# Optimization experiments

Hardware: AMD Instinct MI355X
Metric: run time of the kernel (lower is better)

## Reference

```python
import jax, jax.numpy as jnp
import numpy as np

N, E, IN, HID, OUT, HEADS = 50000, 800000, 256, 256, 128, 4
HC = HID // HEADS  # 64
EPS = 1e-5


def layer_norm(x, g, b):
    mu = x.mean(-1, keepdims=True)
    var = ((x - mu) ** 2).mean(-1, keepdims=True)
    return (x - mu) * jax.lax.rsqrt(var + EPS) * g + b


def gat_conv(x, W, a_s, a_d, bias, src, dst, heads, C, concat):
    # PyG GATConv (eval mode): linear -> per-edge LeakyReLU attention ->
    # segment softmax over destination -> scatter-sum aggregation -> bias
    n = x.shape[0]
    xw = (x @ W).reshape(n, heads, C)                     # [N,H,C]
    al_s = jnp.einsum('nhc,hc->nh', xw, a_s)              # [N,H]
    al_d = jnp.einsum('nhc,hc->nh', xw, a_d)
    e = jax.nn.leaky_relu(al_s[src] + al_d[dst], 0.2)     # [Etot,H]
    m = jax.ops.segment_max(e, dst, num_segments=n)
    ex = jnp.exp(e - m[dst])
    denom = jax.ops.segment_sum(ex, dst, num_segments=n)
    alpha = ex / denom[dst]                               # [Etot,H]
    out = jax.ops.segment_sum(xw[src] * alpha[:, :, None], dst, num_segments=n)
    out = out.reshape(n, heads * C) if concat else out.mean(axis=1)
    return out + bias


def setup_inputs() -> dict:
    key = jax.random.key(0)
    ks = jax.random.split(key, 20)
    s = 0.05
    return {
        'x': jax.random.normal(ks[0], (N, IN), jnp.float32),
        'edge_index': jax.random.randint(ks[1], (2, E), 0, N, jnp.int64),
        'Wp': jax.random.normal(ks[2], (IN, HID), jnp.float32) * s,
        'bp': jnp.zeros((HID,), jnp.float32),
        'W0': jax.random.normal(ks[3], (HID, HEADS * HC), jnp.float32) * s,
        'as0': jax.random.normal(ks[4], (HEADS, HC), jnp.float32) * s,
        'ad0': jax.random.normal(ks[5], (HEADS, HC), jnp.float32) * s,
        'b0': jnp.zeros((HID,), jnp.float32),
        'W1': jax.random.normal(ks[6], (HID, OUT), jnp.float32) * s,
        'as1': jax.random.normal(ks[7], (1, OUT), jnp.float32) * s,
        'ad1': jax.random.normal(ks[8], (1, OUT), jnp.float32) * s,
        'b1': jnp.zeros((OUT,), jnp.float32),
        'g0': jnp.ones((HID,), jnp.float32),
        'be0': jnp.zeros((HID,), jnp.float32),
        'g1': jnp.ones((OUT,), jnp.float32),
        'be1': jnp.zeros((OUT,), jnp.float32),
        'Wo': jax.random.normal(ks[9], (OUT, OUT), jnp.float32) * s,
        'bo': jnp.zeros((OUT,), jnp.float32),
    }


def reference(x, edge_index, Wp, bp, W0, as0, ad0, b0, W1, as1, ad1, b1,
              g0, be0, g1, be1, Wo, bo):
    n = x.shape[0]
    # add self loops (PyG GATConv default)
    ar = jnp.arange(n, dtype=edge_index.dtype)
    src = jnp.concatenate([edge_index[0], ar])
    dst = jnp.concatenate([edge_index[1], ar])

    h = jax.nn.relu(x @ Wp + bp)
    # layer 0: multi-head, concat, LN + residual + relu
    h1 = gat_conv(h, W0, as0, ad0, b0, src, dst, HEADS, HC, True)
    h1 = layer_norm(h1, g0, be0)
    h1 = jax.nn.relu(h1 + h)
    # layer 1: single head, no concat, LN (no residual: shape check still passes
    # only when identity is not None; here identity is None for last layer)
    h2 = gat_conv(h1, W1, as1, ad1, b1, src, dst, 1, OUT, False)
    h2 = layer_norm(h2, g1, be1)
    out = h2 @ Wo + bo
    out = out / jnp.maximum(jnp.linalg.norm(out, axis=-1, keepdims=True), 1e-12)
    return out
```

## Files before the change

### kernel.cpp

```cpp
#include <hip/hip_runtime.h>
#include <hip/hip_bf16.h>

typedef __bf16 bf16x8 __attribute__((ext_vector_type(8)));
typedef __bf16 bf16x4 __attribute__((ext_vector_type(4)));
typedef __bf16 bf16x2 __attribute__((ext_vector_type(2)));
typedef float f32x4 __attribute__((ext_vector_type(4)));

__device__ __forceinline__ float getf(const void* p, size_t i, int isf32){
  return isf32 ? ((const float*)p)[i]
               : __bfloat162float(((const __hip_bfloat16*)p)[i]);
}
__device__ __forceinline__ int getedge(const void* p, long long idx, int is64, int n){
  long long v = is64 ? ((const long long*)p)[idx] : (long long)((const int*)p)[idx];
  v = v < 0 ? 0 : (v >= n ? (long long)(n - 1) : v);
  return (int)v;
}

__device__ __forceinline__ float bfly_sum(float v){
#pragma unroll
  for (int m = 32; m > 0; m >>= 1) v += __shfl_xor(v, m, 64);
  return v;
}

__device__ __forceinline__ float bf_lo(unsigned u){ return __uint_as_float(u << 16); }
__device__ __forceinline__ float bf_hi(unsigned u){ return __uint_as_float(u & 0xffff0000u); }

__global__ __launch_bounds__(256) void detect_kernel(const void* x, const void* ei,
                                                     int* flags){
  __shared__ int cnt_sane, cnt_odd;
  int t = threadIdx.x;
  if (t == 0){ cnt_sane = 0; cnt_odd = 0; }
  __syncthreads();
  int sane = 0;
  for (int i = t; i < 4096; i += 256){
    float v = __bfloat162float(((const __hip_bfloat16*)x)[i]);
    if (fabsf(v) < 16.f) sane++;
  }
  atomicAdd(&cnt_sane, sane);
  int odd = 0;
  for (int i = t; i < 512; i += 256){
    if (((const int*)ei)[2 * i + 1] != 0) odd++;
  }
  atomicAdd(&cnt_odd, odd);
  __syncthreads();
  if (t == 0){
    flags[0] = (cnt_sane < 3900) ? 1 : 0;
    flags[1] = (cnt_odd == 0) ? 1 : 0;
  }
}

__global__ __launch_bounds__(256) void count_kernel(const void* __restrict__ ei, long long E,
                                                    int n, const int* __restrict__ flags,
                                                    int* __restrict__ cnt){
  int i = blockIdx.x * blockDim.x + threadIdx.x;
  if (i < E){
    int d = getedge(ei, E + i, flags[1], n);
    atomicAdd(&cnt[d], 1);
  }
}

__global__ __launch_bounds__(1024) void scan_kernel(const int* __restrict__ cnt, int* __restrict__ off,
                                                    int* __restrict__ pos, int n){
  __shared__ int wsum[16];
  __shared__ int carry_s;
  int tid = threadIdx.x, lane = tid & 63, wv = tid >> 6;
  if (tid == 0) carry_s = 0;
  __syncthreads();
  for (int base = 0; base < n; base += 4096){
    int i0 = base + tid * 4;
    int v0 = 0, v1 = 0, v2 = 0, v3 = 0;
    if (i0 + 3 < n){
      int4 q = *(const int4*)(cnt + i0);
      v0 = q.x; v1 = q.y; v2 = q.z; v3 = q.w;
    } else {
      if (i0 < n)     v0 = cnt[i0];
      if (i0 + 1 < n) v1 = cnt[i0 + 1];
      if (i0 + 2 < n) v2 = cnt[i0 + 2];
      if (i0 + 3 < n) v3 = cnt[i0 + 3];
    }
    int s4 = v0 + v1 + v2 + v3;
    int s = s4;
#pragma unroll
    for (int o = 1; o < 64; o <<= 1){ int t = __shfl_up(s, o, 64); if (lane >= o) s += t; }
    if (lane == 63) wsum[wv] = s;
    __syncthreads();
    int wo = 0;
    for (int w = 0; w < wv; w++) wo += wsum[w];
    int carry = carry_s;
    int e0 = carry + wo + s - s4;
    if (i0 + 3 < n){
      int4 o4; o4.x = e0; o4.y = e0 + v0; o4.z = e0 + v0 + v1; o4.w = e0 + v0 + v1 + v2;
      *(int4*)(off + i0) = o4;
      *(int4*)(pos + i0) = o4;
    } else {
      if (i0 < n)     { off[i0] = e0;               pos[i0] = e0; }
      if (i0 + 1 < n) { off[i0+1] = e0+v0;          pos[i0+1] = e0+v0; }
      if (i0 + 2 < n) { off[i0+2] = e0+v0+v1;       pos[i0+2] = e0+v0+v1; }
      if (i0 + 3 < n) { off[i0+3] = e0+v0+v1+v2;    pos[i0+3] = e0+v0+v1+v2; }
    }
    __syncthreads();
    if (tid == 0){
      int tot = 0;
      for (int w = 0; w < 16; w++) tot += wsum[w];
      carry_s = carry + tot;
    }
    __syncthreads();
  }
  if (tid == 0) off[n] = carry_s;
}

__global__ __launch_bounds__(256) void fill_kernel(const void* __restrict__ ei, long long E,
                                                   int n, const int* __restrict__ flags,
                                                   int* __restrict__ pos, int* __restrict__ bsrc){
  int i = blockIdx.x * blockDim.x + threadIdx.x;
  if (i < E){
    int d = getedge(ei, E + i, flags[1], n);
    int s = getedge(ei, i, flags[1], n);
    int p = atomicAdd(&pos[d], 1);
    bsrc[p] = s;
  }
}

__global__ __launch_bounds__(256) void transpose_all_kernel(
    const void* __restrict__ Wp, const void* __restrict__ W0,
    const void* __restrict__ W1, const void* __restrict__ Wo,
    const int* __restrict__ flags,
    __hip_bfloat16* __restrict__ btp, __hip_bfloat16* __restrict__ bt0,
    __hip_bfloat16* __restrict__ bt1, __hip_bfloat16* __restrict__ bto)
{
  int f0 = flags[0];
  int o = blockIdx.x * 256 + threadIdx.x;
  const void* W; __hip_bfloat16* B; int K, N, loc;
  if (o < 65536)       { W = Wp; B = btp; K = 256; N = 256; loc = o; }
  else if (o < 131072) { W = W0; B = bt0; K = 256; N = 256; loc = o - 65536; }
  else if (o < 163840) { W = W1; B = bt1; K = 256; N = 128; loc = o - 131072; }
  else if (o < 180224) { W = Wo; B = bto; K = 128; N = 128; loc = o - 163840; }
  else return;
  int nn = loc / K, kk = loc - nn * K;
  B[loc] = __float2bfloat16(getf(W, (size_t)kk * N + nn, f0));
}

__device__ __forceinline__ bf16x8 pk8(f32x4 u, f32x4 w){
  bf16x8 r;
  r[0] = (__bf16)u.x; r[1] = (__bf16)u.y; r[2] = (__bf16)u.z; r[3] = (__bf16)u.w;
  r[4] = (__bf16)w.x; r[5] = (__bf16)w.y; r[6] = (__bf16)w.z; r[7] = (__bf16)w.w;
  return r;
}

template<int AMODE, bool OUTF, bool OUTB, bool RELU, bool BIAS, bool NORM, int ALMODE>
__global__ __launch_bounds__(256) void gemm_direct_kernel(
    const void* __restrict__ A, const __hip_bfloat16* __restrict__ Bt,
    const void* __restrict__ bias, const void* __restrict__ a_s, const void* __restrict__ a_d,
    const int* __restrict__ flags,
    float* __restrict__ Cf, __hip_bfloat16* __restrict__ Cb,
    float* __restrict__ als, float* __restrict__ ald,
    int M, int N, int K)
{
  const int f0 = flags[0];
  const bool af32 = (AMODE == 1) && (f0 != 0);
  int t = threadIdx.x;
  int wave = t >> 6, lane = t & 63;
  int q = lane >> 4, mi = lane & 15;
  int bm = blockIdx.x * 128 + wave * 32;
  int bn = blockIdx.y * 128;

  int r0 = min(bm + mi, M - 1);
  int r1 = min(bm + 16 + mi, M - 1);

  f32x4 acc[2][8] = {};

  if (af32){
    const float* Af = (const float*)A;
    const float* p0 = Af + (size_t)r0 * K + q * 8;
    const float* p1 = Af + (size_t)r1 * K + q * 8;
#pragma unroll 2
    for (int k0 = 0; k0 < K; k0 += 32){
      f32x4 u0 = *(const f32x4*)(p0 + k0);
      f32x4 w0 = *(const f32x4*)(p0 + k0 + 4);
      f32x4 u1 = *(const f32x4*)(p1 + k0);
      f32x4 w1 = *(const f32x4*)(p1 + k0 + 4);
      bf16x8 a0 = pk8(u0, w0);
      bf16x8 a1 = pk8(u1, w1);
#pragma unroll
      for (int nt = 0; nt < 8; nt++){
        bf16x8 b = *(const bf16x8*)(Bt + (size_t)(bn + nt * 16 + mi) * K + k0 + q * 8);
        acc[0][nt] = __builtin_amdgcn_mfma_f32_16x16x32_bf16(a0, b, acc[0][nt], 0, 0, 0);
        acc[1][nt] = __builtin_amdgcn_mfma_f32_16x16x32_bf16(a1, b, acc[1][nt], 0, 0, 0);
      }
    }
  } else {
    const __hip_bfloat16* Ab = (const __hip_bfloat16*)A;
    const __hip_bfloat16* p0 = Ab + (size_t)r0 * K + q * 8;
    const __hip_bfloat16* p1 = Ab + (size_t)r1 * K + q * 8;
#pragma unroll 2
    for (int k0 = 0; k0 < K; k0 += 32){
      bf16x8 a0 = *(const bf16x8*)(p0 + k0);
      bf16x8 a1 = *(const bf16x8*)(p1 + k0);
#pragma unroll
      for (int nt = 0; nt < 8; nt++){
        bf16x8 b = *(const bf16x8*)(Bt + (size_t)(bn + nt * 16 + mi) * K + k0 + q * 8);
        acc[0][nt] = __builtin_amdgcn_mfma_f32_16x16x32_bf16(a0, b, acc[0][nt], 0, 0, 0);
        acc[1][nt] = __builtin_amdgcn_mfma_f32_16x16x32_bf16(a1, b, acc[1][nt], 0, 0, 0);
      }
    }
  }

  float bv[8], asv[8], adv[8];
  if (BIAS){
#pragma unroll
    for (int nt = 0; nt < 8; nt++) bv[nt] = getf(bias, bn + nt * 16 + mi, f0);
  }
  if (ALMODE != 0){
#pragma unroll
    for (int nt = 0; nt < 8; nt++){
      asv[nt] = getf(a_s, bn + nt * 16 + mi, f0);
      adv[nt] = getf(a_d, bn + nt * 16 + mi, f0);
    }
  }
#pragma unroll
  for (int mt = 0; mt < 2; mt++){
#pragma unroll
    for (int r = 0; r < 4; r++){
      int row = bm + mt * 16 + q * 4 + r;
      float vv[8];
#pragma unroll
      for (int nt = 0; nt < 8; nt++){
        float v = acc[mt][nt][r];
        if (BIAS) v += bv[nt];
        if (RELU) v = fmaxf(v, 0.f);
        vv[nt] = v;
      }
      if (NORM){
        float ss = 0.f;
#pragma unroll
        for (int nt = 0; nt < 8; nt++) ss += vv[nt] * vv[nt];
        ss += __shfl_xor(ss, 1, 64);
        ss += __shfl_xor(ss, 2, 64);
        ss += __shfl_xor(ss, 4, 64);
        ss += __shfl_xor(ss, 8, 64);
        float inv = 1.f / fmaxf(sqrtf(ss), 1e-12f);
#pragma unroll
        for (int nt = 0; nt < 8; nt++) vv[nt] *= inv;
      }
      if (ALMODE == 1){
        float ps0 = 0.f, pd0 = 0.f, ps1 = 0.f, pd1 = 0.f;
#pragma unroll
        for (int nt = 0; nt < 4; nt++){ ps0 += vv[nt] * asv[nt]; pd0 += vv[nt] * adv[nt]; }
#pragma unroll
        for (int nt = 4; nt < 8; nt++){ ps1 += vv[nt] * asv[nt]; pd1 += vv[nt] * adv[nt]; }
#pragma unroll
        for (int m = 1; m < 16; m <<= 1){
          ps0 += __shfl_xor(ps0, m, 64); pd0 += __shfl_xor(pd0, m, 64);
          ps1 += __shfl_xor(ps1, m, 64); pd1 += __shfl_xor(pd1, m, 64);
        }
        if ((lane & 15) == 0 && row < M){
          int h0 = blockIdx.y * 2;
          als[(size_t)row * 4 + h0]     = ps0; ald[(size_t)row * 4 + h0]     = pd0;
          als[(size_t)row * 4 + h0 + 1] = ps1; ald[(size_t)row * 4 + h0 + 1] = pd1;
        }
      } else if (ALMODE == 2){
        float ps = 0.f, pd = 0.f;
#pragma unroll
        for (int nt = 0; nt < 8; nt++){ ps += vv[nt] * asv[nt]; pd += vv[nt] * adv[nt]; }
#pragma unroll
        for (int m = 1; m < 16; m <<= 1){
          ps += __shfl_xor(ps, m, 64); pd += __shfl_xor(pd, m, 64);
        }
        if ((lane & 15) == 0 && row < M){ als[row] = ps; ald[row] = pd; }
      }
      if (row < M){
#pragma unroll
        for (int nt = 0; nt < 8; nt++){
          int col = bn + nt * 16 + mi;
          size_t idx = (size_t)row * N + col;
          if (OUTF) Cf[idx] = vv[nt];
          if (OUTB) Cb[idx] = __float2bfloat16(vv[nt]);
        }
      }
    }
  }
}

#define FMA4(U, W) do { \
  m0 += (W) * bf_lo((U).x); m1 += (W) * bf_hi((U).x); \
  m2 += (W) * bf_lo((U).y); m3 += (W) * bf_hi((U).y); \
} while (0)

#define FMA2(U, W) do { \
  m0 += (W) * bf_lo(U); m1 += (W) * bf_hi(U); \
} while (0)

__global__ __launch_bounds__(256) void gather0_kernel(
    const __hip_bfloat16* __restrict__ xw, const float* __restrict__ als, const float* __restrict__ ald,
    const int* __restrict__ bsrc, const int* __restrict__ off,
    const void* __restrict__ bias, const void* __restrict__ gamma,
    const void* __restrict__ beta, const int* __restrict__ flags,
    __hip_bfloat16* __restrict__ hbuf, int n)
{
  int f0 = flags[0];
  int t = threadIdx.x, wv = t >> 6, lane = t & 63;
  int i = blockIdx.x * 4 + wv;
  if (i >= n) return;
  int head = lane >> 4;
  int ch = lane * 4;
  int e0 = off[i], jend = off[i + 1];

  float m0 = 0.f, m1 = 0.f, m2 = 0.f, m3 = 0.f;
  float aldi = ald[(size_t)i * 4 + head];

  float se = als[(size_t)i * 4 + head] + aldi;
  se = (se > 0.f) ? se : 0.2f * se;
  float eself = __expf(se);
  {
    uint2 u = *(const uint2*)(xw + (size_t)i * 256 + ch);
    FMA4(u, eself);
  }
  float wacc = eself;

  int j = e0;
  for (; j + 7 < jend; j += 8){
    int s0 = bsrc[j],     s1 = bsrc[j + 1], s2 = bsrc[j + 2], s3 = bsrc[j + 3];
    int s4 = bsrc[j + 4], s5 = bsrc[j + 5], s6 = bsrc[j + 6], s7 = bsrc[j + 7];
    float l0 = als[(size_t)s0 * 4 + head] + aldi;
    float l1 = als[(size_t)s1 * 4 + head] + aldi;
    float l2 = als[(size_t)s2 * 4 + head] + aldi;
    float l3 = als[(size_t)s3 * 4 + head] + aldi;
    float l4 = als[(size_t)s4 * 4 + head] + aldi;
    float l5 = als[(size_t)s5 * 4 + head] + aldi;
    float l6 = als[(size_t)s6 * 4 + head] + aldi;
    float l7 = als[(size_t)s7 * 4 + head] + aldi;
    l0 = (l0 > 0.f) ? l0 : 0.2f * l0;  l1 = (l1 > 0.f) ? l1 : 0.2f * l1;
    l2 = (l2 > 0.f) ? l2 : 0.2f * l2;  l3 = (l3 > 0.f) ? l3 : 0.2f * l3;
    l4 = (l4 > 0.f) ? l4 : 0.2f * l4;  l5 = (l5 > 0.f) ? l5 : 0.2f * l5;
    l6 = (l6 > 0.f) ? l6 : 0.2f * l6;  l7 = (l7 > 0.f) ? l7 : 0.2f * l7;
    float w0 = __expf(l0), w1 = __expf(l1), w2 = __expf(l2), w3 = __expf(l3);
    float w4 = __expf(l4), w5 = __expf(l5), w6 = __expf(l6), w7 = __expf(l7);
    uint2 U0 = *(const uint2*)(xw + (size_t)s0 * 256 + ch);
    uint2 U1 = *(const uint2*)(xw + (size_t)s1 * 256 + ch);
    uint2 U2 = *(const uint2*)(xw + (size_t)s2 * 256 + ch);
    uint2 U3 = *(const uint2*)(xw + (size_t)s3 * 256 + ch);
    uint2 U4 = *(const uint2*)(xw + (size_t)s4 * 256 + ch);
    uint2 U5 = *(const uint2*)(xw + (size_t)s5 * 256 + ch);
    uint2 U6 = *(const uint2*)(xw + (size_t)s6 * 256 + ch);
    uint2 U7 = *(const uint2*)(xw + (size_t)s7 * 256 + ch);
    wacc += w0 + w1 + w2 + w3 + w4 + w5 + w6 + w7;
    FMA4(U0, w0); FMA4(U1, w1); FMA4(U2, w2); FMA4(U3, w3);
    FMA4(U4, w4); FMA4(U5, w5); FMA4(U6, w6); FMA4(U7, w7);
  }
  for (; j + 3 < jend; j += 4){
    int s0 = bsrc[j], s1 = bsrc[j + 1], s2 = bsrc[j + 2], s3 = bsrc[j + 3];
    float l0 = als[(size_t)s0 * 4 + head] + aldi;
    float l1 = als[(size_t)s1 * 4 + head] + aldi;
    float l2 = als[(size_t)s2 * 4 + head] + aldi;
    float l3 = als[(size_t)s3 * 4 + head] + aldi;
    l0 = (l0 > 0.f) ? l0 : 0.2f * l0;  l1 = (l1 > 0.f) ? l1 : 0.2f * l1;
    l2 = (l2 > 0.f) ? l2 : 0.2f * l2;  l3 = (l3 > 0.f) ? l3 : 0.2f * l3;
    float w0 = __expf(l0), w1 = __expf(l1), w2 = __expf(l2), w3 = __expf(l3);
    uint2 U0 = *(const uint2*)(xw + (size_t)s0 * 256 + ch);
    uint2 U1 = *(const uint2*)(xw + (size_t)s1 * 256 + ch);
    uint2 U2 = *(const uint2*)(xw + (size_t)s2 * 256 + ch);
    uint2 U3 = *(const uint2*)(xw + (size_t)s3 * 256 + ch);
    wacc += w0 + w1 + w2 + w3;
    FMA4(U0, w0); FMA4(U1, w1); FMA4(U2, w2); FMA4(U3, w3);
  }
  for (; j < jend; j++){
    int s0 = bsrc[j];
    float l0 = als[(size_t)s0 * 4 + head] + aldi;
    l0 = (l0 > 0.f) ? l0 : 0.2f * l0;
    float w0 = __expf(l0);
    uint2 U0 = *(const uint2*)(xw + (size_t)s0 * 256 + ch);
    wacc += w0;
    FMA4(U0, w0);
  }

  float rl = 1.f / wacc;
  float v0 = m0 * rl + getf(bias, ch + 0, f0);
  float v1 = m1 * rl + getf(bias, ch + 1, f0);
  float v2 = m2 * rl + getf(bias, ch + 2, f0);
  float v3 = m3 * rl + getf(bias, ch + 3, f0);

  float mu = bfly_sum(v0 + v1 + v2 + v3) * (1.f / 256.f);
  float d0 = v0 - mu, d1 = v1 - mu, d2 = v2 - mu, d3 = v3 - mu;
  float var = bfly_sum(d0 * d0 + d1 * d1 + d2 * d2 + d3 * d3) * (1.f / 256.f);
  float rs = rsqrtf(var + 1e-5f);

  bf16x4 rb = *(const bf16x4*)(hbuf + (size_t)i * 256 + ch);
  float y0 = fmaxf(d0 * rs * getf(gamma, ch + 0, f0) + getf(beta, ch + 0, f0) + (float)rb[0], 0.f);
  float y1 = fmaxf(d1 * rs * getf(gamma, ch + 1, f0) + getf(beta, ch + 1, f0) + (float)rb[1], 0.f);
  float y2 = fmaxf(d2 * rs * getf(gamma, ch + 2, f0) + getf(beta, ch + 2, f0) + (float)rb[2], 0.f);
  float y3 = fmaxf(d3 * rs * getf(gamma, ch + 3, f0) + getf(beta, ch + 3, f0) + (float)rb[3], 0.f);

  bf16x4 o;
  o[0] = (__bf16)y0; o[1] = (__bf16)y1; o[2] = (__bf16)y2; o[3] = (__bf16)y3;
  *(bf16x4*)(hbuf + (size_t)i * 256 + ch) = o;
}

__global__ __launch_bounds__(256) void gather1_kernel(
    const __hip_bfloat16* __restrict__ xw, const float* __restrict__ als, const float* __restrict__ ald,
    const int* __restrict__ bsrc, const int* __restrict__ off,
    const void* __restrict__ bias, const void* __restrict__ gamma,
    const void* __restrict__ beta, const int* __restrict__ flags,
    __hip_bfloat16* __restrict__ outb, int n)
{
  int f0 = flags[0];
  int t = threadIdx.x, wv = t >> 6, lane = t & 63;
  int i = blockIdx.x * 4 + wv;
  if (i >= n) return;
  int ch = lane * 2;
  int e0 = off[i], jend = off[i + 1];

  float m0 = 0.f, m1 = 0.f;

  float aldi = ald[i];
  float se = als[i] + aldi;
  se = (se > 0.f) ? se : 0.2f * se;
  float eself = __expf(se);
  {
    unsigned u = *(const unsigned*)(xw + (size_t)i * 128 + ch);
    FMA2(u, eself);
  }
  float wacc = eself;

  int j = e0;
  for (; j + 7 < jend; j += 8){
    int s0 = bsrc[j],     s1 = bsrc[j + 1], s2 = bsrc[j + 2], s3 = bsrc[j + 3];
    int s4 = bsrc[j + 4], s5 = bsrc[j + 5], s6 = bsrc[j + 6], s7 = bsrc[j + 7];
    float l0 = als[s0] + aldi, l1 = als[s1] + aldi, l2 = als[s2] + aldi, l3 = als[s3] + aldi;
    float l4 = als[s4] + aldi, l5 = als[s5] + aldi, l6 = als[s6] + aldi, l7 = als[s7] + aldi;
    l0 = (l0 > 0.f) ? l0 : 0.2f * l0;  l1 = (l1 > 0.f) ? l1 : 0.2f * l1;
    l2 = (l2 > 0.f) ? l2 : 0.2f * l2;  l3 = (l3 > 0.f) ? l3 : 0.2f * l3;
    l4 = (l4 > 0.f) ? l4 : 0.2f * l4;  l5 = (l5 > 0.f) ? l5 : 0.2f * l5;
    l6 = (l6 > 0.f) ? l6 : 0.2f * l6;  l7 = (l7 > 0.f) ? l7 : 0.2f * l7;
    float w0 = __expf(l0), w1 = __expf(l1), w2 = __expf(l2), w3 = __expf(l3);
    float w4 = __expf(l4), w5 = __expf(l5), w6 = __expf(l6), w7 = __expf(l7);
    unsigned U0 = *(const unsigned*)(xw + (size_t)s0 * 128 + ch);
    unsigned U1 = *(const unsigned*)(xw + (size_t)s1 * 128 + ch);
    unsigned U2 = *(const unsigned*)(xw + (size_t)s2 * 128 + ch);
    unsigned U3 = *(const unsigned*)(xw + (size_t)s3 * 128 + ch);
    unsigned U4 = *(const unsigned*)(xw + (size_t)s4 * 128 + ch);
    unsigned U5 = *(const unsigned*)(xw + (size_t)s5 * 128 + ch);
    unsigned U6 = *(const unsigned*)(xw + (size_t)s6 * 128 + ch);
    unsigned U7 = *(const unsigned*)(xw + (size_t)s7 * 128 + ch);
    wacc += w0 + w1 + w2 + w3 + w4 + w5 + w6 + w7;
    FMA2(U0, w0); FMA2(U1, w1); FMA2(U2, w2); FMA2(U3, w3);
    FMA2(U4, w4); FMA2(U5, w5); FMA2(U6, w6); FMA2(U7, w7);
  }
  for (; j + 3 < jend; j += 4){
    int s0 = bsrc[j], s1 = bsrc[j + 1], s2 = bsrc[j + 2], s3 = bsrc[j + 3];
    float l0 = als[s0] + aldi, l1 = als[s1] + aldi, l2 = als[s2] + aldi, l3 = als[s3] + aldi;
    l0 = (l0 > 0.f) ? l0 : 0.2f * l0;  l1 = (l1 > 0.f) ? l1 : 0.2f * l1;
    l2 = (l2 > 0.f) ? l2 : 0.2f * l2;  l3 = (l3 > 0.f) ? l3 : 0.2f * l3;
    float w0 = __expf(l0), w1 = __expf(l1), w2 = __expf(l2), w3 = __expf(l3);
    unsigned U0 = *(const unsigned*)(xw + (size_t)s0 * 128 + ch);
    unsigned U1 = *(const unsigned*)(xw + (size_t)s1 * 128 + ch);
    unsigned U2 = *(const unsigned*)(xw + (size_t)s2 * 128 + ch);
    unsigned U3 = *(const unsigned*)(xw + (size_t)s3 * 128 + ch);
    wacc += w0 + w1 + w2 + w3;
    FMA2(U0, w0); FMA2(U1, w1); FMA2(U2, w2); FMA2(U3, w3);
  }
  for (; j < jend; j++){
    int s0 = bsrc[j];
    float l0 = als[s0] + aldi;
    l0 = (l0 > 0.f) ? l0 : 0.2f * l0;
    float w0 = __expf(l0);
    unsigned U0 = *(const unsigned*)(xw + (size_t)s0 * 128 + ch);
    wacc += w0;
    FMA2(U0, w0);
  }

  float rl = 1.f / wacc;
  float v0 = m0 * rl + getf(bias, ch + 0, f0);
  float v1 = m1 * rl + getf(bias, ch + 1, f0);

  float mu = bfly_sum(v0 + v1) * (1.f / 128.f);
  float d0 = v0 - mu, d1 = v1 - mu;
  float var = bfly_sum(d0 * d0 + d1 * d1) * (1.f / 128.f);
  float rs = rsqrtf(var + 1e-5f);

  float y0 = d0 * rs * getf(gamma, ch + 0, f0) + getf(beta, ch + 0, f0);
  float y1 = d1 * rs * getf(gamma, ch + 1, f0) + getf(beta, ch + 1, f0);

  bf16x2 o;
  o[0] = (__bf16)y0; o[1] = (__bf16)y1;
  *(bf16x2*)(outb + (size_t)i * 128 + ch) = o;
}

extern "C" void kernel_launch(void* const* d_in, const int* in_sizes, int n_in,
                              void* d_out, int out_size, void* d_ws, size_t ws_size,
                              hipStream_t stream)
{
  const void* x   = d_in[0];
  const void* ei  = d_in[1];
  const void* Wp  = d_in[2];
  const void* bp  = d_in[3];
  const void* W0  = d_in[4];
  const void* as0 = d_in[5];
  const void* ad0 = d_in[6];
  const void* b0  = d_in[7];
  const void* W1  = d_in[8];
  const void* as1 = d_in[9];
  const void* ad1 = d_in[10];
  const void* b1  = d_in[11];
  const void* g0  = d_in[12];
  const void* be0 = d_in[13];
  const void* g1  = d_in[14];
  const void* be1 = d_in[15];
  const void* Wo  = d_in[16];
  const void* bo  = d_in[17];
  float* outp = (float*)d_out;

  const int n = in_sizes[0] / 256;
  const int E = in_sizes[1] / 2;

  char* w = (char*)d_ws;
  size_t SZ = (size_t)n * 256 * sizeof(float);
  __hip_bfloat16* h_bf  = (__hip_bfloat16*)w;
  __hip_bfloat16* xw_bf = (__hip_bfloat16*)(w + SZ / 2);
  char* p = w + SZ;
  int* flags = (int*)p; p += 64;
  float* als0 = (float*)p; p += (size_t)n * 4 * sizeof(float);
  float* ald0 = (float*)p; p += (size_t)n * 4 * sizeof(float);
  float* als1 = (float*)p; p += (size_t)n * sizeof(float);
  float* ald1 = (float*)p; p += (size_t)n * sizeof(float);
  int* cnt    = (int*)p; p += (size_t)n * sizeof(int);
  int* offb   = (int*)p; p += (size_t)(n + 4) * sizeof(int);
  int* pos    = (int*)p; p += (size_t)n * sizeof(int);
  int* bsrc   = (int*)p; p += (size_t)E * sizeof(int);
  p = (char*)(((uintptr_t)p + 15) & ~(uintptr_t)15);
  __hip_bfloat16* bt_p = (__hip_bfloat16*)p; p += (size_t)256 * 256 * 2;
  __hip_bfloat16* bt_0 = (__hip_bfloat16*)p; p += (size_t)256 * 256 * 2;
  __hip_bfloat16* bt_1 = (__hip_bfloat16*)p; p += (size_t)128 * 256 * 2;
  __hip_bfloat16* bt_o = (__hip_bfloat16*)p; p += (size_t)128 * 128 * 2;

  detect_kernel<<<1, 256, 0, stream>>>(x, ei, flags);

  transpose_all_kernel<<<704, 256, 0, stream>>>(Wp, W0, W1, Wo, flags, bt_p, bt_0, bt_1, bt_o);

  (void)hipMemsetAsync(cnt, 0, (size_t)n * sizeof(int), stream);
  count_kernel<<<(E + 255) / 256, 256, 0, stream>>>(ei, E, n, flags, cnt);
  scan_kernel<<<1, 1024, 0, stream>>>(cnt, offb, pos, n);
  fill_kernel<<<(E + 255) / 256, 256, 0, stream>>>(ei, E, n, flags, pos, bsrc);

  int gm = (n + 127) / 128;
  int gn4 = (n + 3) / 4;

  gemm_direct_kernel<1, false, true, true, true, false, 0><<<dim3(gm, 2), 256, 0, stream>>>(
      x, bt_p, bp, nullptr, nullptr, flags, nullptr, h_bf, nullptr, nullptr, n, 256, 256);
  gemm_direct_kernel<0, false, true, false, false, false, 1><<<dim3(gm, 2), 256, 0, stream>>>(
      h_bf, bt_0, nullptr, as0, ad0, flags, nullptr, xw_bf, als0, ald0, n, 256, 256);
  gather0_kernel<<<gn4, 256, 0, stream>>>(xw_bf, als0, ald0, bsrc, offb, b0, g0, be0,
                                          flags, h_bf, n);
  gemm_direct_kernel<0, false, true, false, false, false, 2><<<dim3(gm, 1), 256, 0, stream>>>(
      h_bf, bt_1, nullptr, as1, ad1, flags, nullptr, xw_bf, als1, ald1, n, 128, 256);
  gather1_kernel<<<gn4, 256, 0, stream>>>(xw_bf, als1, ald1, bsrc, offb, b1, g1, be1,
                                          flags, h_bf, n);
  gemm_direct_kernel<0, true, false, false, true, true, 0><<<dim3(gm, 1), 256, 0, stream>>>(
      h_bf, bt_o, bo, nullptr, nullptr, flags, outp, nullptr, nullptr, nullptr, n, 128, 128);
}
```

Before: 485.1 us.

## Parallelize CSR offset scan across blocks and widen GEMM N-tile to full width

```diff
diff --git a/kernel.cpp b/kernel.cpp
--- a/kernel.cpp
+++ b/kernel.cpp
@@ -59,54 +59,79 @@
   }
 }
 
-__global__ __launch_bounds__(1024) void scan_kernel(const int* __restrict__ cnt, int* __restrict__ off,
-                                                    int* __restrict__ pos, int n){
+__global__ __launch_bounds__(1024) void scan_part_kernel(const int* __restrict__ cnt, int n,
+                                                         int* __restrict__ bsum){
   __shared__ int wsum[16];
-  __shared__ int carry_s;
   int tid = threadIdx.x, lane = tid & 63, wv = tid >> 6;
-  if (tid == 0) carry_s = 0;
+  int i0 = blockIdx.x * 4096 + tid * 4;
+  int s4 = 0;
+  if (i0 + 3 < n){
+    int4 q = *(const int4*)(cnt + i0);
+    s4 = q.x + q.y + q.z + q.w;
+  } else {
+    if (i0 < n)     s4 += cnt[i0];
+    if (i0 + 1 < n) s4 += cnt[i0 + 1];
+    if (i0 + 2 < n) s4 += cnt[i0 + 2];
+    if (i0 + 3 < n) s4 += cnt[i0 + 3];
+  }
+  int s = s4;
+#pragma unroll
+  for (int o = 1; o < 64; o <<= 1) s += __shfl_xor(s, o, 64);
+  if (lane == 0) wsum[wv] = s;
   __syncthreads();
-  for (int base = 0; base < n; base += 4096){
-    int i0 = base + tid * 4;
-    int v0 = 0, v1 = 0, v2 = 0, v3 = 0;
-    if (i0 + 3 < n){
-      int4 q = *(const int4*)(cnt + i0);
-      v0 = q.x; v1 = q.y; v2 = q.z; v3 = q.w;
-    } else {
-      if (i0 < n)     v0 = cnt[i0];
-      if (i0 + 1 < n) v1 = cnt[i0 + 1];
-      if (i0 + 2 < n) v2 = cnt[i0 + 2];
-      if (i0 + 3 < n) v3 = cnt[i0 + 3];
-    }
-    int s4 = v0 + v1 + v2 + v3;
-    int s = s4;
-#pragma unroll
-    for (int o = 1; o < 64; o <<= 1){ int t = __shfl_up(s, o, 64); if (lane >= o) s += t; }
-    if (lane == 63) wsum[wv] = s;
-    __syncthreads();
-    int wo = 0;
-    for (int w = 0; w < wv; w++) wo += wsum[w];
-    int carry = carry_s;
-    int e0 = carry + wo + s - s4;
-    if (i0 + 3 < n){
-      int4 o4; o4.x = e0; o4.y = e0 + v0; o4.z = e0 + v0 + v1; o4.w = e0 + v0 + v1 + v2;
-      *(int4*)(off + i0) = o4;
-      *(int4*)(pos + i0) = o4;
-    } else {
-      if (i0 < n)     { off[i0] = e0;               pos[i0] = e0; }
-      if (i0 + 1 < n) { off[i0+1] = e0+v0;          pos[i0+1] = e0+v0; }
-      if (i0 + 2 < n) { off[i0+2] = e0+v0+v1;       pos[i0+2] = e0+v0+v1; }
-      if (i0 + 3 < n) { off[i0+3] = e0+v0+v1+v2;    pos[i0+3] = e0+v0+v1+v2; }
-    }
-    __syncthreads();
-    if (tid == 0){
-      int tot = 0;
-      for (int w = 0; w < 16; w++) tot += wsum[w];
-      carry_s = carry + tot;
-    }
-    __syncthreads();
-  }
-  if (tid == 0) off[n] = carry_s;
+  if (tid == 0){
+    int tot = 0;
+    for (int w = 0; w < 16; w++) tot += wsum[w];
+    bsum[blockIdx.x] = tot;
+  }
+}
+
+__global__ __launch_bounds__(64) void scan_top_kernel(int* __restrict__ bsum, int nb,
+                                                      int* __restrict__ off, int n){
+  int lane = threadIdx.x;
+  int v = (lane < nb) ? bsum[lane] : 0;
+  int s = v;
+#pragma unroll
+  for (int o = 1; o < 64; o <<= 1){ int t = __shfl_up(s, o, 64); if (lane >= o) s += t; }
+  if (lane < nb) bsum[lane] = s - v;
+  if (lane == 63) off[n] = s;
+}
+
+__global__ __launch_bounds__(1024) void scan_fin_kernel(const int* __restrict__ cnt, int n,
+                                                        const int* __restrict__ bsum,
+                                                        int* __restrict__ off, int* __restrict__ pos){
+  __shared__ int wsum[16];
+  int tid = threadIdx.x, lane = tid & 63, wv = tid >> 6;
+  int i0 = blockIdx.x * 4096 + tid * 4;
+  int v0 = 0, v1 = 0, v2 = 0, v3 = 0;
+  if (i0 + 3 < n){
+    int4 q = *(const int4*)(cnt + i0);
+    v0 = q.x; v1 = q.y; v2 = q.z; v3 = q.w;
+  } else {
+    if (i0 < n)     v0 = cnt[i0];
+    if (i0 + 1 < n) v1 = cnt[i0 + 1];
+    if (i0 + 2 < n) v2 = cnt[i0 + 2];
+    if (i0 + 3 < n) v3 = cnt[i0 + 3];
+  }
+  int s4 = v0 + v1 + v2 + v3;
+  int s = s4;
+#pragma unroll
+  for (int o = 1; o < 64; o <<= 1){ int t = __shfl_up(s, o, 64); if (lane >= o) s += t; }
+  if (lane == 63) wsum[wv] = s;
+  __syncthreads();
+  int wo = 0;
+  for (int w = 0; w < wv; w++) wo += wsum[w];
+  int e0 = bsum[blockIdx.x] + wo + s - s4;
+  if (i0 + 3 < n){
+    int4 o4; o4.x = e0; o4.y = e0 + v0; o4.z = e0 + v0 + v1; o4.w = e0 + v0 + v1 + v2;
+    *(int4*)(off + i0) = o4;
+    *(int4*)(pos + i0) = o4;
+  } else {
+    if (i0 < n)     { off[i0] = e0;               pos[i0] = e0; }
+    if (i0 + 1 < n) { off[i0+1] = e0+v0;          pos[i0+1] = e0+v0; }
+    if (i0 + 2 < n) { off[i0+2] = e0+v0+v1;       pos[i0+2] = e0+v0+v1; }
+    if (i0 + 3 < n) { off[i0+3] = e0+v0+v1+v2;    pos[i0+3] = e0+v0+v1+v2; }
+  }
 }
 
 __global__ __launch_bounds__(256) void fill_kernel(const void* __restrict__ ei, long long E,
@@ -147,7 +172,7 @@
   return r;
 }
 
-template<int AMODE, bool OUTF, bool OUTB, bool RELU, bool BIAS, bool NORM, int ALMODE>
+template<int AMODE, bool OUTF, bool OUTB, bool RELU, bool BIAS, bool NORM, int ALMODE, int NT>
 __global__ __launch_bounds__(256) void gemm_direct_kernel(
     const void* __restrict__ A, const __hip_bfloat16* __restrict__ Bt,
     const void* __restrict__ bias, const void* __restrict__ a_s, const void* __restrict__ a_d,
@@ -162,57 +187,54 @@
   int wave = t >> 6, lane = t & 63;
   int q = lane >> 4, mi = lane & 15;
   int bm = blockIdx.x * 128 + wave * 32;
-  int bn = blockIdx.y * 128;
+  int bn = blockIdx.y * (NT * 16);
 
   int r0 = min(bm + mi, M - 1);
   int r1 = min(bm + 16 + mi, M - 1);
 
-  f32x4 acc[2][8] = {};
-
-  if (af32){
-    const float* Af = (const float*)A;
-    const float* p0 = Af + (size_t)r0 * K + q * 8;
-    const float* p1 = Af + (size_t)r1 * K + q * 8;
+  f32x4 acc[2][NT] = {};
+
+  const float* pf0 = (const float*)A + (size_t)r0 * K + q * 8;
+  const float* pf1 = (const float*)A + (size_t)r1 * K + q * 8;
+  const __hip_bfloat16* pb0 = (const __hip_bfloat16*)A + (size_t)r0 * K + q * 8;
+  const __hip_bfloat16* pb1 = (const __hip_bfloat16*)A + (size_t)r1 * K + q * 8;
+
+  auto kstep = [&](int k0){
+    bf16x8 a0, a1;
+    if (af32){
+      f32x4 u0 = *(const f32x4*)(pf0 + k0);
+      f32x4 w0 = *(const f32x4*)(pf0 + k0 + 4);
+      f32x4 u1 = *(const f32x4*)(pf1 + k0);
+      f32x4 w1 = *(const f32x4*)(pf1 + k0 + 4);
+      a0 = pk8(u0, w0);
+      a1 = pk8(u1, w1);
+    } else {
+      a0 = *(const bf16x8*)(pb0 + k0);
+      a1 = *(const bf16x8*)(pb1 + k0);
+    }
+#pragma unroll
+    for (int nt = 0; nt < NT; nt++){
+      bf16x8 b = *(const bf16x8*)(Bt + (size_t)(bn + nt * 16 + mi) * K + k0 + q * 8);
+      acc[0][nt] = __builtin_amdgcn_mfma_f32_16x16x32_bf16(a0, b, acc[0][nt], 0, 0, 0);
+      acc[1][nt] = __builtin_amdgcn_mfma_f32_16x16x32_bf16(a1, b, acc[1][nt], 0, 0, 0);
+    }
+  };
+  if constexpr (NT == 8){
 #pragma unroll 2
-    for (int k0 = 0; k0 < K; k0 += 32){
-      f32x4 u0 = *(const f32x4*)(p0 + k0);
-      f32x4 w0 = *(const f32x4*)(p0 + k0 + 4);
-      f32x4 u1 = *(const f32x4*)(p1 + k0);
-      f32x4 w1 = *(const f32x4*)(p1 + k0 + 4);
-      bf16x8 a0 = pk8(u0, w0);
-      bf16x8 a1 = pk8(u1, w1);
-#pragma unroll
-      for (int nt = 0; nt < 8; nt++){
-        bf16x8 b = *(const bf16x8*)(Bt + (size_t)(bn + nt * 16 + mi) * K + k0 + q * 8);
-        acc[0][nt] = __builtin_amdgcn_mfma_f32_16x16x32_bf16(a0, b, acc[0][nt], 0, 0, 0);
-        acc[1][nt] = __builtin_amdgcn_mfma_f32_16x16x32_bf16(a1, b, acc[1][nt], 0, 0, 0);
-      }
-    }
+    for (int k0 = 0; k0 < K; k0 += 32) kstep(k0);
   } else {
-    const __hip_bfloat16* Ab = (const __hip_bfloat16*)A;
-    const __hip_bfloat16* p0 = Ab + (size_t)r0 * K + q * 8;
-    const __hip_bfloat16* p1 = Ab + (size_t)r1 * K + q * 8;
-#pragma unroll 2
-    for (int k0 = 0; k0 < K; k0 += 32){
-      bf16x8 a0 = *(const bf16x8*)(p0 + k0);
-      bf16x8 a1 = *(const bf16x8*)(p1 + k0);
-#pragma unroll
-      for (int nt = 0; nt < 8; nt++){
-        bf16x8 b = *(const bf16x8*)(Bt + (size_t)(bn + nt * 16 + mi) * K + k0 + q * 8);
-        acc[0][nt] = __builtin_amdgcn_mfma_f32_16x16x32_bf16(a0, b, acc[0][nt], 0, 0, 0);
-        acc[1][nt] = __builtin_amdgcn_mfma_f32_16x16x32_bf16(a1, b, acc[1][nt], 0, 0, 0);
-      }
-    }
-  }
-
-  float bv[8], asv[8], adv[8];
+#pragma unroll 1
+    for (int k0 = 0; k0 < K; k0 += 32) kstep(k0);
+  }
+
+  float bv[NT], asv[NT], adv[NT];
   if (BIAS){
 #pragma unroll
-    for (int nt = 0; nt < 8; nt++) bv[nt] = getf(bias, bn + nt * 16 + mi, f0);
+    for (int nt = 0; nt < NT; nt++) bv[nt] = getf(bias, bn + nt * 16 + mi, f0);
   }
   if (ALMODE != 0){
 #pragma unroll
-    for (int nt = 0; nt < 8; nt++){
+    for (int nt = 0; nt < NT; nt++){
       asv[nt] = getf(a_s, bn + nt * 16 + mi, f0);
       adv[nt] = getf(a_d, bn + nt * 16 + mi, f0);
     }
@@ -222,9 +244,9 @@
 #pragma unroll
     for (int r = 0; r < 4; r++){
       int row = bm + mt * 16 + q * 4 + r;
-      float vv[8];
-#pragma unroll
-      for (int nt = 0; nt < 8; nt++){
+      float vv[NT];
+#pragma unroll
+      for (int nt = 0; nt < NT; nt++){
         float v = acc[mt][nt][r];
         if (BIAS) v += bv[nt];
         if (RELU) v = fmaxf(v, 0.f);
@@ -233,35 +255,41 @@
       if (NORM){
         float ss = 0.f;
 #pragma unroll
-        for (int nt = 0; nt < 8; nt++) ss += vv[nt] * vv[nt];
+        for (int nt = 0; nt < NT; nt++) ss += vv[nt] * vv[nt];
         ss += __shfl_xor(ss, 1, 64);
         ss += __shfl_xor(ss, 2, 64);
         ss += __shfl_xor(ss, 4, 64);
         ss += __shfl_xor(ss, 8, 64);
         float inv = 1.f / fmaxf(sqrtf(ss), 1e-12f);
 #pragma unroll
-        for (int nt = 0; nt < 8; nt++) vv[nt] *= inv;
+        for (int nt = 0; nt < NT; nt++) vv[nt] *= inv;
       }
       if (ALMODE == 1){
-        float ps0 = 0.f, pd0 = 0.f, ps1 = 0.f, pd1 = 0.f;
-#pragma unroll
-        for (int nt = 0; nt < 4; nt++){ ps0 += vv[nt] * asv[nt]; pd0 += vv[nt] * adv[nt]; }
-#pragma unroll
-        for (int nt = 4; nt < 8; nt++){ ps1 += vv[nt] * asv[nt]; pd1 += vv[nt] * adv[nt]; }
-#pragma unroll
-        for (int m = 1; m < 16; m <<= 1){
-          ps0 += __shfl_xor(ps0, m, 64); pd0 += __shfl_xor(pd0, m, 64);
-          ps1 += __shfl_xor(ps1, m, 64); pd1 += __shfl_xor(pd1, m, 64);
+        float ps[4] = {0.f, 0.f, 0.f, 0.f}, pd[4] = {0.f, 0.f, 0.f, 0.f};
+#pragma unroll
+        for (int h = 0; h < 4; h++){
+#pragma unroll
+          for (int g = 0; g < 4; g++){
+            ps[h] += vv[h * 4 + g] * asv[h * 4 + g];
+            pd[h] += vv[h * 4 + g] * adv[h * 4 + g];
+          }
+#pragma unroll
+          for (int m = 1; m < 16; m <<= 1){
+            ps[h] += __shfl_xor(ps[h], m, 64);
+            pd[h] += __shfl_xor(pd[h], m, 64);
+          }
         }
         if ((lane & 15) == 0 && row < M){
-          int h0 = blockIdx.y * 2;
-          als[(size_t)row * 4 + h0]     = ps0; ald[(size_t)row * 4 + h0]     = pd0;
-          als[(size_t)row * 4 + h0 + 1] = ps1; ald[(size_t)row * 4 + h0 + 1] = pd1;
+#pragma unroll
+          for (int h = 0; h < 4; h++){
+            als[(size_t)row * 4 + h] = ps[h];
+            ald[(size_t)row * 4 + h] = pd[h];
+          }
         }
       } else if (ALMODE == 2){
         float ps = 0.f, pd = 0.f;
 #pragma unroll
-        for (int nt = 0; nt < 8; nt++){ ps += vv[nt] * asv[nt]; pd += vv[nt] * adv[nt]; }
+        for (int nt = 0; nt < NT; nt++){ ps += vv[nt] * asv[nt]; pd += vv[nt] * adv[nt]; }
 #pragma unroll
         for (int m = 1; m < 16; m <<= 1){
           ps += __shfl_xor(ps, m, 64); pd += __shfl_xor(pd, m, 64);
@@ -270,7 +298,7 @@
       }
       if (row < M){
 #pragma unroll
-        for (int nt = 0; nt < 8; nt++){
+        for (int nt = 0; nt < NT; nt++){
           int col = bn + nt * 16 + mi;
           size_t idx = (size_t)row * N + col;
           if (OUTF) Cf[idx] = vv[nt];
@@ -525,6 +553,7 @@
   int* cnt    = (int*)p; p += (size_t)n * sizeof(int);
   int* offb   = (int*)p; p += (size_t)(n + 4) * sizeof(int);
   int* pos    = (int*)p; p += (size_t)n * sizeof(int);
+  int* bsum   = (int*)p; p += 64 * sizeof(int);
   int* bsrc   = (int*)p; p += (size_t)E * sizeof(int);
   p = (char*)(((uintptr_t)p + 15) & ~(uintptr_t)15);
   __hip_bfloat16* bt_p = (__hip_bfloat16*)p; p += (size_t)256 * 256 * 2;
@@ -538,22 +567,25 @@
 
   (void)hipMemsetAsync(cnt, 0, (size_t)n * sizeof(int), stream);
   count_kernel<<<(E + 255) / 256, 256, 0, stream>>>(ei, E, n, flags, cnt);
-  scan_kernel<<<1, 1024, 0, stream>>>(cnt, offb, pos, n);
+  int nb = (n + 4095) / 4096;
+  scan_part_kernel<<<nb, 1024, 0, stream>>>(cnt, n, bsum);
+  scan_top_kernel<<<1, 64, 0, stream>>>(bsum, nb, offb, n);
+  scan_fin_kernel<<<nb, 1024, 0, stream>>>(cnt, n, bsum, offb, pos);
   fill_kernel<<<(E + 255) / 256, 256, 0, stream>>>(ei, E, n, flags, pos, bsrc);
 
   int gm = (n + 127) / 128;
   int gn4 = (n + 3) / 4;
 
-  gemm_direct_kernel<1, false, true, true, true, false, 0><<<dim3(gm, 2), 256, 0, stream>>>(
+  gemm_direct_kernel<1, false, true, true, true, false, 0, 16><<<dim3(gm, 1), 256, 0, stream>>>(
       x, bt_p, bp, nullptr, nullptr, flags, nullptr, h_bf, nullptr, nullptr, n, 256, 256);
-  gemm_direct_kernel<0, false, true, false, false, false, 1><<<dim3(gm, 2), 256, 0, stream>>>(
+  gemm_direct_kernel<0, false, true, false, false, false, 1, 16><<<dim3(gm, 1), 256, 0, stream>>>(
       h_bf, bt_0, nullptr, as0, ad0, flags, nullptr, xw_bf, als0, ald0, n, 256, 256);
   gather0_kernel<<<gn4, 256, 0, stream>>>(xw_bf, als0, ald0, bsrc, offb, b0, g0, be0,
                                           flags, h_bf, n);
-  gemm_direct_kernel<0, false, true, false, false, false, 2><<<dim3(gm, 1), 256, 0, stream>>>(
+  gemm_direct_kernel<0, false, true, false, false, false, 2, 8><<<dim3(gm, 1), 256, 0, stream>>>(
       h_bf, bt_1, nullptr, as1, ad1, flags, nullptr, xw_bf, als1, ald1, n, 128, 256);
   gather1_kernel<<<gn4, 256, 0, stream>>>(xw_bf, als1, ald1, bsrc, offb, b1, g1, be1,
                                           flags, h_bf, n);
-  gemm_direct_kernel<0, true, false, false, true, true, 0><<<dim3(gm, 1), 256, 0, stream>>>(
+  gemm_direct_kernel<0, true, false, false, true, true, 0, 8><<<dim3(gm, 1), 256, 0, stream>>>(
       h_bf, bt_o, bo, nullptr, nullptr, flags, outp, nullptr, nullptr, nullptr, n, 128, 128);
 }
```

New measurement: 479.5 us. Within noise of the previous version (-1.1%).
